# Kernel tuning notes

Measured on AMD Instinct MI355X. Metric: run time of the kernel, lower is better.

The kernel has to match this reference:

```python
import jax, jax.numpy as jnp
import numpy as np

H_BINS = 61
INSZ = 150
EPS = 1e-6


def rgb_uv_hist(img, sigma_u, sigma_v, c):
    """Differentiable RGB-uv soft histogram with per-channel RBF kernels.
    img: [B,3,H,W] in [0,1]; sigma_u, sigma_v, c: [3]. Returns [B,3,h,h]."""
    B = img.shape[0]
    x = jnp.clip(img, 0.0, 1.0).reshape(B, 3, -1)          # [B,3,P]
    Iy = jnp.sqrt(jnp.sum(x * x, axis=1))                  # [B,P] intensity weight
    lg = jnp.log(x + EPS)
    # log-chromaticity (u,v) per reference channel c in {R,G,B}
    u = jnp.stack([lg[:, 0] - lg[:, 1], lg[:, 1] - lg[:, 0], lg[:, 2] - lg[:, 0]], 1)  # [B,3,P]
    v = jnp.stack([lg[:, 0] - lg[:, 2], lg[:, 1] - lg[:, 2], lg[:, 2] - lg[:, 1]], 1)
    bins = jnp.linspace(-3.0, 3.0, H_BINS).astype(img.dtype)
    ku = jnp.exp(-((u[..., None] - bins) ** 2) / (sigma_u[None, :, None, None] ** 2))  # [B,3,P,h]
    kv = jnp.exp(-((v[..., None] - bins) ** 2) / (sigma_v[None, :, None, None] ** 2))
    w = Iy[:, None, :] * c[None, :, None]                  # [B,3,P]
    hist = jnp.einsum('bcpu,bcp,bcpv->bcuv', ku, w, kv)    # [B,3,h,h]
    norm = jnp.sum(hist, axis=(1, 2, 3), keepdims=True) + EPS
    return hist / norm


def _conv(x, w, b, stride):
    y = jax.lax.conv_general_dilated(x, w, (stride, stride), 'VALID',
                                     dimension_numbers=('NCHW', 'OIHW', 'NCHW'))
    return jax.nn.relu(y + b[None, :, None, None])


def _head(hist, w1, b1, w2, b2, w3, b3, fc):
    z = _conv(hist, w1, b1, 2)   # 61 -> 29
    z = _conv(z, w2, b2, 2)      # 29 -> 14
    z = _conv(z, w3, b3, 1)      # 14 -> 13
    z = z.reshape(z.shape[0], -1)  # [B, 512*13*13]
    return jnp.abs(z @ fc.T)


def setup_inputs() -> dict:
    key = jax.random.key(0)
    ks = jax.random.split(key, 16)
    B = 16
    d = {}
    d['image'] = jax.random.uniform(ks[0], (B, 3, INSZ, INSZ), jnp.float32)
    # hist params: sigmas in a numerically reasonable range (orig init: random()*0.02)
    d['su_s'] = 0.05 + 0.2 * jax.random.uniform(ks[1], (3,), jnp.float32)
    d['sv_s'] = 0.05 + 0.2 * jax.random.uniform(ks[2], (3,), jnp.float32)
    d['c_s'] = jnp.ones((3,), jnp.float32)
    d['w1_s'] = 0.05 * jax.random.normal(ks[3], (128, 3, 5, 5), jnp.float32)
    d['b1_s'] = jnp.zeros((128,), jnp.float32)
    d['w2_s'] = 0.02 * jax.random.normal(ks[4], (256, 128, 3, 3), jnp.float32)
    d['b2_s'] = jnp.zeros((256,), jnp.float32)
    d['w3_s'] = 0.02 * jax.random.normal(ks[5], (512, 256, 2, 2), jnp.float32)
    d['b3_s'] = jnp.zeros((512,), jnp.float32)
    d['fc_s'] = 0.003 * jax.random.normal(ks[6], (9, 512 * 13 * 13), jnp.float32)
    d['su_i'] = 0.05 + 0.2 * jax.random.uniform(ks[7], (3,), jnp.float32)
    d['sv_i'] = 0.05 + 0.2 * jax.random.uniform(ks[8], (3,), jnp.float32)
    d['c_i'] = jnp.ones((3,), jnp.float32)
    d['w1_i'] = 0.05 * jax.random.normal(ks[9], (128, 3, 5, 5), jnp.float32)
    d['b1_i'] = jnp.zeros((128,), jnp.float32)
    d['w2_i'] = 0.02 * jax.random.normal(ks[10], (256, 128, 3, 3), jnp.float32)
    d['b2_i'] = jnp.zeros((256,), jnp.float32)
    d['w3_i'] = 0.02 * jax.random.normal(ks[11], (512, 256, 2, 2), jnp.float32)
    d['b3_i'] = jnp.zeros((512,), jnp.float32)
    d['fc_i'] = 0.003 * jax.random.normal(ks[12], (3, 512 * 13 * 13), jnp.float32)
    return d


def reference(image, su_s, sv_s, c_s, w1_s, b1_s, w2_s, b2_s, w3_s, b3_s, fc_s,
              su_i, sv_i, c_i, w1_i, b1_i, w2_i, b2_i, w3_i, b3_i, fc_i):
    B = image.shape[0]
    # sensor branch: hist -> CNN -> |fc| -> 3x3 matrix (transposed), L1-row-norm scaled
    hs = rgb_uv_hist(image, su_s, sv_s, c_s)
    m = _head(hs, w1_s, b1_s, w2_s, b2_s, w3_s, b3_s, fc_s).reshape(B, 3, 3)
    m = jnp.swapaxes(m, -1, -2)                               # .t()
    n = jnp.max(jnp.sum(jnp.abs(m), axis=-1), axis=-1) + 1e-4  # max L1 row norm, [B]
    m = m / n[:, None, None]
    # color mapping: pixels @ m^T
    mapped = jnp.einsum('bjhw,bij->bihw', image, m)
    # illuminant branch on mapped image
    hi = rgb_uv_hist(mapped, su_i, sv_i, c_i)
    ill = _head(hi, w1_i, b1_i, w2_i, b2_i, w3_i, b3_i, fc_i)  # [B,3]
    est_ill = jnp.einsum('bij,bj->bi', jnp.linalg.inv(m), ill)
    return est_ill
```

## Files before the change

kernel.cpp:

```cpp
#include <hip/hip_runtime.h>

#define P_PIX 22500
#define HB 61
#define HSP 30
#define PPB 768
#define NCHK 6

typedef float f32x4 __attribute__((ext_vector_type(4)));
typedef _Float16 f16x8 __attribute__((ext_vector_type(8)));
typedef _Float16 f16x4 __attribute__((ext_vector_type(4)));

static __device__ __forceinline__ unsigned pk2(float a, float b)
{
    return __builtin_bit_cast(unsigned, __builtin_amdgcn_cvt_pkrtz(a, b));
}

static __device__ __forceinline__ float exp2_hw(float x)
{
    return __builtin_amdgcn_exp2f(x);
}

__global__ __launch_bounds__(256) void hist_mfma(
    const float* __restrict__ img, const float* __restrict__ su,
    const float* __restrict__ sv, const float* __restrict__ cw,
    const float* __restrict__ msc, float* __restrict__ hpart)
{
    const int bc = blockIdx.x;
    const int b = bc / 3, c = bc % 3;
    const int split = blockIdx.y;
    const int tid  = threadIdx.x;
    const int wv   = tid >> 6;
    const int lane = tid & 63;
    const int quad = lane >> 4;
    const int mr   = lane & 15;

    __shared__ __align__(16) _Float16 B_lds[8192];
    __shared__ __align__(16) float su_l[PPB];
    __shared__ __align__(16) float sv_l[PPB];
    __shared__ __align__(16) float sw_l[PPB];

    const float sig_u = su[c], sig_v = sv[c];
    const float L2E = 1.4426950408889634f;
    const float c1u = -L2E / (sig_u * sig_u);
    const float c1v = -L2E / (sig_v * sig_v);
    const float cwc = cw[c];
    const float ubin_b = -3.f + 0.1f * (float)lane;
    const float ubin_a = -3.f + 0.1f * (float)(wv * 16 + mr);

    const bool hasM = (msc != nullptr);
    float m00=0,m01=0,m02=0,m10=0,m11=0,m12=0,m20=0,m21=0,m22=0;
    if (hasM) {
        const float* mp = msc + b * 9;
        m00=mp[0]; m01=mp[1]; m02=mp[2];
        m10=mp[3]; m11=mp[4]; m12=mp[5];
        m20=mp[6]; m21=mp[7]; m22=mp[8];
    }

    const int p0 = split * PPB;

    for (int i = tid; i < PPB; i += 256) {
        int px = p0 + i;
        float u = 0.f, v = 0.f, wgt = 0.f;
        if (px < P_PIX) {
            const float* ip = img + (size_t)b * 3 * P_PIX + px;
            float r = ip[0], g = ip[P_PIX], bl = ip[2 * P_PIX];
            if (hasM) {
                float r2 = m00 * r + m01 * g + m02 * bl;
                float g2 = m10 * r + m11 * g + m12 * bl;
                float b2 = m20 * r + m21 * g + m22 * bl;
                r = r2; g = g2; bl = b2;
            }
            r  = fminf(fmaxf(r, 0.f), 1.f);
            g  = fminf(fmaxf(g, 0.f), 1.f);
            bl = fminf(fmaxf(bl, 0.f), 1.f);
            float Iy = sqrtf(r * r + g * g + bl * bl);
            float lr = __logf(r + 1e-6f);
            float lg = __logf(g + 1e-6f);
            float lb = __logf(bl + 1e-6f);
            if (c == 0)      { u = lr - lg; v = lr - lb; }
            else if (c == 1) { u = lg - lr; v = lg - lb; }
            else             { u = lb - lr; v = lb - lg; }
            wgt = Iy * cwc;
        }
        su_l[i] = u; sv_l[i] = v; sw_l[i] = wgt;
    }
    __syncthreads();

    f32x4 acc[4];
#pragma unroll
    for (int nt = 0; nt < 4; ++nt) acc[nt] = (f32x4){0.f, 0.f, 0.f, 0.f};

    for (int chunk = 0; chunk < NCHK; ++chunk) {
        const float* suc = &su_l[chunk * 128];
        const float* svc = &sv_l[chunk * 128];
        const float* swc = &sw_l[chunk * 128];

#pragma unroll
        for (int r = 0; r < 4; ++r) {
            int pg = wv + 4 * r;
            f32x4 v0 = *(const f32x4*)&svc[pg * 8];
            f32x4 v1 = *(const f32x4*)&svc[pg * 8 + 4];
            float e[8];
#pragma unroll
            for (int j = 0; j < 4; ++j) {
                float d0 = v0[j] - ubin_b;
                e[j] = exp2_hw((d0 * c1v) * d0);
                float d1 = v1[j] - ubin_b;
                e[4 + j] = exp2_hw((d1 * c1v) * d1);
            }
            union { f16x8 h; unsigned w[4]; } bv;
            bv.w[0] = pk2(e[0], e[1]);
            bv.w[1] = pk2(e[2], e[3]);
            bv.w[2] = pk2(e[4], e[5]);
            bv.w[3] = pk2(e[6], e[7]);
            *(f16x8*)&B_lds[(pg * 64 + lane) * 8] = bv.h;
        }
        f16x8 af[4];
#pragma unroll
        for (int kk = 0; kk < 4; ++kk) {
            int pxg = kk * 4 + quad;
            f32x4 u0 = *(const f32x4*)&suc[pxg * 8];
            f32x4 u1 = *(const f32x4*)&suc[pxg * 8 + 4];
            f32x4 w0 = *(const f32x4*)&swc[pxg * 8];
            f32x4 w1 = *(const f32x4*)&swc[pxg * 8 + 4];
            float e[8];
#pragma unroll
            for (int j = 0; j < 4; ++j) {
                float d0 = u0[j] - ubin_a;
                e[j] = exp2_hw((d0 * c1u) * d0) * w0[j];
                float d1 = u1[j] - ubin_a;
                e[4 + j] = exp2_hw((d1 * c1u) * d1) * w1[j];
            }
            union { f16x8 h; unsigned w[4]; } av;
            av.w[0] = pk2(e[0], e[1]);
            av.w[1] = pk2(e[2], e[3]);
            av.w[2] = pk2(e[4], e[5]);
            av.w[3] = pk2(e[6], e[7]);
            af[kk] = av.h;
        }
        __syncthreads();
#pragma unroll
        for (int kk = 0; kk < 4; ++kk) {
            int pgq = kk * 4 + quad;
#pragma unroll
            for (int nt = 0; nt < 4; ++nt) {
                f16x8 bvv = *(const f16x8*)&B_lds[(pgq * 64 + nt * 16 + mr) * 8];
                acc[nt] = __builtin_amdgcn_mfma_f32_16x16x32_f16(af[kk], bvv, acc[nt], 0, 0, 0);
            }
        }
        __syncthreads();
    }

    float* hp = hpart + ((size_t)bc * HSP + split) * 4096;
#pragma unroll
    for (int nt = 0; nt < 4; ++nt) {
        int v = nt * 16 + mr;
#pragma unroll
        for (int r = 0; r < 4; ++r) {
            int u = wv * 16 + quad * 4 + r;
            hp[u * 64 + v] = acc[nt][r];
        }
    }
}

__global__ __launch_bounds__(256) void reduce_hist(
    const float* __restrict__ hpart, float* __restrict__ hist,
    float* __restrict__ hsum3)
{
    const int bc = blockIdx.x;
    const int part = blockIdx.y;
    const int tid = threadIdx.x;
    const float* base = hpart + (size_t)bc * HSP * 4096;
    float lsum = 0.f;
#pragma unroll
    for (int t = 0; t < 4; ++t) {
        int idx = part * 1024 + t * 256 + tid;
        int u = idx >> 6, v = idx & 63;
        float s = 0.f;
        for (int sp = 0; sp < HSP; ++sp) s += base[sp * 4096 + idx];
        if (u < HB && v < HB) {
            hist[(size_t)bc * (HB * HB) + u * HB + v] = s;
            lsum += s;
        }
    }
    __shared__ float red[4];
    for (int off = 32; off; off >>= 1) lsum += __shfl_down(lsum, off, 64);
    if ((tid & 63) == 0) red[tid >> 6] = lsum;
    __syncthreads();
    if (tid == 0) atomicAdd(&hsum3[bc], red[0] + red[1] + red[2] + red[3]);
}

__global__ __launch_bounds__(256) void conv1_mfma(
    const float* __restrict__ hist, const float* __restrict__ hsum3,
    const _Float16* __restrict__ w1h, const float* __restrict__ bias,
    _Float16* __restrict__ out)
{
    const int b    = blockIdx.x;
    const int m0   = blockIdx.y * 64;
    const int tid  = threadIdx.x;
    const int wv   = tid >> 6;
    const int lane = tid & 63;
    const int quad = lane >> 4;
    const int mr   = lane & 15;

    __shared__ __align__(16) _Float16 A_lds[64 * 96];

    const float sc = 1.f / (hsum3[b * 3] + hsum3[b * 3 + 1] + hsum3[b * 3 + 2] + 1e-6f);
    const float* inb = hist + (size_t)b * 3 * 3721;

    for (int slot = tid; slot < 768; slot += 256) {
        int m  = slot & 63;
        int kg = slot >> 6;
        int mg = m0 + m;
        bool mok = (mg < 841);
        int oh = mok ? mg / 29 : 0;
        int ow = mok ? mg % 29 : 0;
        const float* pbase = inb + (oh * 2) * 61 + (ow * 2);
        f16x8 av;
#pragma unroll
        for (int j = 0; j < 8; ++j) {
            int k = kg * 8 + j;
            float x = 0.f;
            if (mok && k < 75) {
                int ci = k / 25, r = k % 25;
                int kh = r / 5, kw = r % 5;
                x = pbase[ci * 3721 + kh * 61 + kw] * sc;
            }
            av[j] = (_Float16)x;
        }
        *(f16x8*)&A_lds[(kg * 64 + m) * 8] = av;
    }
    __syncthreads();

    f16x8 wf[3][2];
#pragma unroll
    for (int ks = 0; ks < 3; ++ks)
#pragma unroll
        for (int nt = 0; nt < 2; ++nt) {
            int co = (wv * 2 + nt) * 16 + mr;
            wf[ks][nt] = *(const f16x8*)&w1h[co * 96 + ks * 32 + quad * 8];
        }

    f32x4 acc[4][2];
#pragma unroll
    for (int mt = 0; mt < 4; ++mt)
#pragma unroll
        for (int nt = 0; nt < 2; ++nt) acc[mt][nt] = (f32x4){0.f, 0.f, 0.f, 0.f};

#pragma unroll
    for (int ks = 0; ks < 3; ++ks)
#pragma unroll
        for (int mt = 0; mt < 4; ++mt) {
            f16x8 bv = *(const f16x8*)&A_lds[((ks * 4 + quad) * 64 + mt * 16 + mr) * 8];
#pragma unroll
            for (int nt = 0; nt < 2; ++nt)
                acc[mt][nt] = __builtin_amdgcn_mfma_f32_16x16x32_f16(bv, wf[ks][nt], acc[mt][nt], 0, 0, 0);
        }

#pragma unroll
    for (int mt = 0; mt < 4; ++mt) {
#pragma unroll
        for (int r = 0; r < 4; ++r) {
            int sp = m0 + mt * 16 + quad * 4 + r;
            if (sp >= 841) continue;
#pragma unroll
            for (int nt = 0; nt < 2; ++nt) {
                int co = (wv * 2 + nt) * 16 + mr;
                float y = acc[mt][nt][r] + bias[co];
                out[((size_t)b * 841 + sp) * 128 + co] = (_Float16)fmaxf(y, 0.f);
            }
        }
    }
}

template<int CIN, int COUT, int Kk, int S, int IN, int OUT,
         int NPB, int KSPL, int KCH, int MTILE>
__global__ __launch_bounds__(256) void conv_mfma(
    const _Float16* __restrict__ in_h,
    const _Float16* __restrict__ w_h,
    float* __restrict__ out)
{
    constexpr int KK   = Kk * Kk;
    constexpr int OSZ  = OUT * OUT;
    constexpr int MP   = MTILE;
    constexpr int MT   = MTILE / 16;
    constexpr int KTOT = CIN * KK;
    constexpr int KC   = KTOT / KSPL;
    constexpr int NCHUNK = KC / KCH;
    constexpr int NT   = NPB / 64;
    constexpr int NSPL = COUT / NPB;
    constexpr int KSN  = KCH / 32;
    constexpr int SLOTS = MP * (KCH / 8);

    const int b    = blockIdx.x;
    const int m0   = (blockIdx.y / NSPL) * MTILE;
    const int co0  = (blockIdx.y % NSPL) * NPB;
    const int k00  = blockIdx.z * KC;
    const int tid  = threadIdx.x;
    const int wv   = tid >> 6;
    const int lane = tid & 63;
    const int quad = lane >> 4;
    const int mr   = lane & 15;

    __shared__ __align__(16) _Float16 A_lds[MP * KCH];

    const _Float16* inb = in_h + (size_t)b * (IN * IN) * CIN;
    float* outp = out + (size_t)blockIdx.z * gridDim.x * OSZ * COUT;

    f32x4 acc[MT][NT];
#pragma unroll
    for (int mt = 0; mt < MT; ++mt)
#pragma unroll
        for (int nt = 0; nt < NT; ++nt) acc[mt][nt] = (f32x4){0.f, 0.f, 0.f, 0.f};

    for (int ch = 0; ch < NCHUNK; ++ch) {
        const int k0 = k00 + ch * KCH;
        __syncthreads();
        for (int slot = tid; slot < SLOTS; slot += 256) {
            int m  = slot % MP;
            int kg = slot / MP;
            int mg = m0 + m;
            bool mok = (mg < OSZ);
            int oh = mok ? mg / OUT : 0;
            int ow = mok ? mg % OUT : 0;
            int kbase = k0 + kg * 8;
            int khkw = kbase / CIN;
            int ci0  = kbase % CIN;
            int kh = khkw / Kk, kw = khkw % Kk;
            f16x8 av = (f16x8)(_Float16)0.f;
            if (mok)
                av = *(const f16x8*)&inb[((size_t)((oh * S + kh) * IN + (ow * S + kw))) * CIN + ci0];
            *(f16x8*)&A_lds[(kg * MP + m) * 8] = av;
        }
        __syncthreads();
        f16x8 wf[KSN][NT];
#pragma unroll
        for (int ks = 0; ks < KSN; ++ks)
#pragma unroll
            for (int nt = 0; nt < NT; ++nt) {
                int co = co0 + (wv * NT + nt) * 16 + mr;
                wf[ks][nt] = *(const f16x8*)&w_h[(size_t)co * KTOT + k0 + ks * 32 + quad * 8];
            }
#pragma unroll
        for (int ks = 0; ks < KSN; ++ks) {
#pragma unroll
            for (int mt = 0; mt < MT; ++mt) {
                f16x8 bv = *(const f16x8*)&A_lds[((ks * 4 + quad) * MP + mt * 16 + mr) * 8];
#pragma unroll
                for (int nt = 0; nt < NT; ++nt)
                    acc[mt][nt] = __builtin_amdgcn_mfma_f32_16x16x32_f16(bv, wf[ks][nt], acc[mt][nt], 0, 0, 0);
            }
        }
    }

#pragma unroll
    for (int mt = 0; mt < MT; ++mt) {
#pragma unroll
        for (int r = 0; r < 4; ++r) {
            int sp = m0 + mt * 16 + quad * 4 + r;
            if (sp >= OSZ) continue;
#pragma unroll
            for (int nt = 0; nt < NT; ++nt) {
                int co = co0 + (wv * NT + nt) * 16 + mr;
                outp[((size_t)b * OSZ + sp) * COUT + co] = acc[mt][nt][r];
            }
        }
    }
}

__global__ __launch_bounds__(256) void reduce_bias_relu_f16(
    const float* __restrict__ p, const float* __restrict__ bias,
    _Float16* __restrict__ out, int cout, int total4, int kspl, int total)
{
    for (int i4 = blockIdx.x * 256 + threadIdx.x; i4 < total4; i4 += gridDim.x * 256) {
        f32x4 s = (f32x4){0.f, 0.f, 0.f, 0.f};
        for (int ks = 0; ks < kspl; ++ks)
            s += *(const f32x4*)&p[(size_t)ks * total + i4 * 4];
        f32x4 bb = *(const f32x4*)&bias[(i4 * 4) % cout];
        f16x4 o;
#pragma unroll
        for (int j = 0; j < 4; ++j) o[j] = (_Float16)fmaxf(s[j] + bb[j], 0.f);
        *(f16x4*)&out[(size_t)i4 * 4] = o;
    }
}

__global__ __launch_bounds__(256) void fc_mfma(
    const _Float16* __restrict__ z, const _Float16* __restrict__ fcw,
    float* __restrict__ out, int NO)
{
    const int tid  = threadIdx.x;
    const int wv   = tid >> 6;
    const int lane = tid & 63;
    const int quad = lane >> 4;
    const int mr   = lane & 15;
    const int kw0  = blockIdx.x * 512 + wv * 128;

    __shared__ float sred[1024];

    f32x4 acc = (f32x4){0.f, 0.f, 0.f, 0.f};
    const bool bok = (mr < NO);
#pragma unroll
    for (int ks = 0; ks < 4; ++ks) {
        int kk = kw0 + ks * 32 + quad * 8;
        f16x8 av = *(const f16x8*)&z[(size_t)mr * 86528 + kk];
        f16x8 bw = (f16x8)(_Float16)0.f;
        if (bok) bw = *(const f16x8*)&fcw[(size_t)mr * 86528 + kk];
        acc = __builtin_amdgcn_mfma_f32_16x16x32_f16(av, bw, acc, 0, 0, 0);
    }
#pragma unroll
    for (int r = 0; r < 4; ++r)
        sred[wv * 256 + (quad * 4 + r) * 16 + mr] = acc[r];
    __syncthreads();
    if (tid < 256) {
        float s = sred[tid] + sred[256 + tid] + sred[512 + tid] + sred[768 + tid];
        int o = tid & 15, b = tid >> 4;
        if (o < NO) atomicAdd(&out[b * NO + o], s);
    }
}

__global__ __launch_bounds__(256) void prep_weights(
    const float* __restrict__ w1s, const float* __restrict__ w1i,
    const float* __restrict__ w2s, const float* __restrict__ w3s,
    const float* __restrict__ w2i, const float* __restrict__ w3i,
    const float* __restrict__ fcs, const float* __restrict__ fci,
    _Float16* __restrict__ w1h, _Float16* __restrict__ w23,
    _Float16* __restrict__ fch, float* __restrict__ zp)
{
    const int R0 = 384;
    const int R1 = 24576;
    const int N2 = 294912, N3 = 524288;
    const int R2 = 2 * (N2 + N3);
    const int K = 86528;
    const int R3 = 12 * K;
    const int T = R0 + R1 + R2 + R3;
    for (int i = blockIdx.x * 256 + threadIdx.x; i < T; i += gridDim.x * 256) {
        if (i < R0) {
            zp[i] = 0.f;
        } else if (i < R0 + R1) {
            int r0 = i - R0;
            int br = r0 / 12288, r = r0 % 12288;
            int co = r / 96, k = r % 96;
            const float* s = br ? w1i : w1s;
            w1h[r0] = (k < 75) ? (_Float16)s[co * 75 + k] : (_Float16)0.f;
        } else if (i < R0 + R1 + R2) {
            int j = i - R0 - R1;
            int out_idx = j;
            const float* s; int CK, KKn;
            if (j < N2)                { s = w2s; CK = 1152; KKn = 9; }
            else if (j < N2 + N3)      { s = w3s; j -= N2; CK = 1024; KKn = 4; }
            else if (j < 2 * N2 + N3)  { s = w2i; j -= N2 + N3; CK = 1152; KKn = 9; }
            else                       { s = w3i; j -= 2 * N2 + N3; CK = 1024; KKn = 4; }
            int co = j / CK, rem = j % CK;
            int ci = rem % (CK / KKn), khkw = rem / (CK / KKn);
            w23[out_idx] = (_Float16)s[co * CK + ci * KKn + khkw];
        } else {
            int j = i - R0 - R1 - R2;
            int o = j / K, rem = j % K;
            int sp = rem / 512, co = rem % 512;
            const float* s = (o < 9) ? (fcs + o * K) : (fci + (o - 9) * K);
            fch[j] = (_Float16)s[co * 169 + sp];
        }
    }
}

__global__ void build_m(const float* __restrict__ h, float* __restrict__ msc)
{
    int b = threadIdx.x;
    if (b < 16) {
        float m[9];
#pragma unroll
        for (int i = 0; i < 3; ++i)
#pragma unroll
            for (int j = 0; j < 3; ++j) m[i * 3 + j] = fabsf(h[b * 9 + j * 3 + i]);
        float n = 0.f;
#pragma unroll
        for (int i = 0; i < 3; ++i) {
            float r = m[i * 3] + m[i * 3 + 1] + m[i * 3 + 2];
            n = fmaxf(n, r);
        }
        n += 1e-4f;
        float inv = 1.f / n;
#pragma unroll
        for (int k = 0; k < 9; ++k) msc[b * 9 + k] = m[k] * inv;
    }
}

__global__ void final_est(const float* __restrict__ msc, const float* __restrict__ ill,
                          float* __restrict__ out)
{
    int bidx = threadIdx.x;
    if (bidx < 16) {
        const float* m = msc + bidx * 9;
        float a = m[0], b = m[1], c = m[2];
        float d = m[3], e = m[4], f = m[5];
        float g = m[6], h = m[7], i = m[8];
        float A = e * i - f * h, B = f * g - d * i, C = d * h - e * g;
        float D = c * h - b * i, E = a * i - c * g, F = b * g - a * h;
        float G = b * f - c * e, H = c * d - a * f, I = a * e - b * d;
        float det = a * A + b * B + c * C;
        float inv_det = 1.f / det;
        float x0 = fabsf(ill[bidx * 3 + 0]);
        float x1 = fabsf(ill[bidx * 3 + 1]);
        float x2 = fabsf(ill[bidx * 3 + 2]);
        out[bidx * 3 + 0] = (A * x0 + D * x1 + G * x2) * inv_det;
        out[bidx * 3 + 1] = (B * x0 + E * x1 + H * x2) * inv_det;
        out[bidx * 3 + 2] = (C * x0 + F * x1 + I * x2) * inv_det;
    }
}

extern "C" void kernel_launch(void* const* d_in, const int* in_sizes, int n_in,
                              void* d_out, int out_size, void* d_ws, size_t ws_size,
                              hipStream_t stream)
{
    (void)in_sizes; (void)n_in; (void)out_size; (void)ws_size;
    const float* image = (const float*)d_in[0];
    const float* su_s  = (const float*)d_in[1];
    const float* sv_s  = (const float*)d_in[2];
    const float* c_s   = (const float*)d_in[3];
    const float* w1_s  = (const float*)d_in[4];
    const float* b1_s  = (const float*)d_in[5];
    const float* w2_s  = (const float*)d_in[6];
    const float* b2_s  = (const float*)d_in[7];
    const float* w3_s  = (const float*)d_in[8];
    const float* b3_s  = (const float*)d_in[9];
    const float* fc_s  = (const float*)d_in[10];
    const float* su_i  = (const float*)d_in[11];
    const float* sv_i  = (const float*)d_in[12];
    const float* c_i   = (const float*)d_in[13];
    const float* w1_i  = (const float*)d_in[14];
    const float* b1_i  = (const float*)d_in[15];
    const float* w2_i  = (const float*)d_in[16];
    const float* b2_i  = (const float*)d_in[17];
    const float* w3_i  = (const float*)d_in[18];
    const float* b3_i  = (const float*)d_in[19];
    const float* fc_i  = (const float*)d_in[20];

    float* W      = (float*)d_ws;
    float* hist   = W;
    float* hd     = hist + 178608;
    float* hd2    = hd + 144;
    float* hsum3a = hd2 + 144;
    float* hsum3b = hsum3a + 48;
    float* msc    = hsum3b + 48;
    float* U      = msc + 144;
    float* hpart  = U;
    float* p2     = U;
    float* p3     = U;
    _Float16* o1h   = (_Float16*)(U + 11075584);
    _Float16* o2h   = o1h   + 1722368;
    _Float16* o3h   = o2h   + 802816;
    _Float16* fch   = o3h   + 1384448;
    _Float16* w2h_s = fch   + 1038336;
    _Float16* w3h_s = w2h_s + 294912;
    _Float16* w2h_i = w3h_s + 524288;
    _Float16* w3h_i = w2h_i + 294912;
    _Float16* w1h_s = w3h_i + 524288;
    _Float16* w1h_i = w1h_s + 12288;

    const int O2_TOT = 16 * 196 * 256;
    const int O3_TOT = 16 * 169 * 512;
    const int FCK = 86528;

    prep_weights<<<1024, 256, 0, stream>>>(w1_s, w1_i, w2_s, w3_s, w2_i, w3_i,
                                           fc_s, fc_i, w1h_s, w2h_s, fch, hd);

    hist_mfma<<<dim3(48, HSP), 256, 0, stream>>>(image, su_s, sv_s, c_s, nullptr, hpart);
    reduce_hist<<<dim3(48, 4), 256, 0, stream>>>(hpart, hist, hsum3a);
    conv1_mfma<<<dim3(16, 14), 256, 0, stream>>>(hist, hsum3a, w1h_s, b1_s, o1h);
    conv_mfma<128, 256, 3, 2, 29, 14, 128, 4, 96, 112><<<dim3(16, 4, 4), 256, 0, stream>>>(o1h, w2h_s, p2);
    reduce_bias_relu_f16<<<784, 256, 0, stream>>>(p2, b2_s, o2h, 256, O2_TOT / 4, 4, O2_TOT);
    conv_mfma<256, 512, 2, 1, 14, 13, 128, 2, 64, 96><<<dim3(16, 8, 2), 256, 0, stream>>>(o2h, w3h_s, p3);
    reduce_bias_relu_f16<<<1024, 256, 0, stream>>>(p3, b3_s, o3h, 512, O3_TOT / 4, 2, O3_TOT);
    fc_mfma<<<169, 256, 0, stream>>>(o3h, fch, hd, 9);
    build_m<<<1, 64, 0, stream>>>(hd, msc);

    hist_mfma<<<dim3(48, HSP), 256, 0, stream>>>(image, su_i, sv_i, c_i, msc, hpart);
    reduce_hist<<<dim3(48, 4), 256, 0, stream>>>(hpart, hist, hsum3b);
    conv1_mfma<<<dim3(16, 14), 256, 0, stream>>>(hist, hsum3b, w1h_i, b1_i, o1h);
    conv_mfma<128, 256, 3, 2, 29, 14, 128, 4, 96, 112><<<dim3(16, 4, 4), 256, 0, stream>>>(o1h, w2h_i, p2);
    reduce_bias_relu_f16<<<784, 256, 0, stream>>>(p2, b2_i, o2h, 256, O2_TOT / 4, 4, O2_TOT);
    conv_mfma<256, 512, 2, 1, 14, 13, 128, 2, 64, 96><<<dim3(16, 8, 2), 256, 0, stream>>>(o2h, w3h_i, p3);
    reduce_bias_relu_f16<<<1024, 256, 0, stream>>>(p3, b3_i, o3h, 512, O3_TOT / 4, 2, O3_TOT);
    fc_mfma<<<169, 256, 0, stream>>>(o3h, fch + 9 * FCK, hd2, 3);
    final_est<<<1, 64, 0, stream>>>(msc, hd2, (float*)d_out);
}
```

Measured before the change: 327.5 us.

## Fuse bias+ReLU into conv2/conv3 MFMA kernels and drop split-K partials

Removes the split-K decomposition of the conv2 and conv3 MFMA kernels, so each block accumulates the full K range and applies bias and ReLU before writing f16 output directly. This eliminates the fp32 partial-sum buffers and the separate reduce_bias_relu kernels, cutting four launches and their global memory round-trips. Tiles shrink to 64 output channels and 64 spatial rows per block to keep enough blocks in the grid without split-K. In exchange, each block runs a longer serial K loop and reuses the A tile across fewer output channels.

```diff
diff --git a/kernel.cpp b/kernel.cpp
--- a/kernel.cpp
+++ b/kernel.cpp
@@ -274,20 +274,19 @@
 }
 
 template<int CIN, int COUT, int Kk, int S, int IN, int OUT,
-         int NPB, int KSPL, int KCH, int MTILE>
-__global__ __launch_bounds__(256) void conv_mfma(
+         int NPB, int KCH, int MTILE>
+__global__ __launch_bounds__(256) void conv_fused_mfma(
     const _Float16* __restrict__ in_h,
     const _Float16* __restrict__ w_h,
-    float* __restrict__ out)
+    const float* __restrict__ bias,
+    _Float16* __restrict__ out)
 {
     constexpr int KK   = Kk * Kk;
     constexpr int OSZ  = OUT * OUT;
     constexpr int MP   = MTILE;
     constexpr int MT   = MTILE / 16;
     constexpr int KTOT = CIN * KK;
-    constexpr int KC   = KTOT / KSPL;
-    constexpr int NCHUNK = KC / KCH;
-    constexpr int NT   = NPB / 64;
+    constexpr int NCHUNK = KTOT / KCH;
     constexpr int NSPL = COUT / NPB;
     constexpr int KSN  = KCH / 32;
     constexpr int SLOTS = MP * (KCH / 8);
@@ -295,7 +294,6 @@
     const int b    = blockIdx.x;
     const int m0   = (blockIdx.y / NSPL) * MTILE;
     const int co0  = (blockIdx.y % NSPL) * NPB;
-    const int k00  = blockIdx.z * KC;
     const int tid  = threadIdx.x;
     const int wv   = tid >> 6;
     const int lane = tid & 63;
@@ -305,16 +303,13 @@
     __shared__ __align__(16) _Float16 A_lds[MP * KCH];
 
     const _Float16* inb = in_h + (size_t)b * (IN * IN) * CIN;
-    float* outp = out + (size_t)blockIdx.z * gridDim.x * OSZ * COUT;
-
-    f32x4 acc[MT][NT];
-#pragma unroll
-    for (int mt = 0; mt < MT; ++mt)
-#pragma unroll
-        for (int nt = 0; nt < NT; ++nt) acc[mt][nt] = (f32x4){0.f, 0.f, 0.f, 0.f};
+
+    f32x4 acc[MT];
+#pragma unroll
+    for (int mt = 0; mt < MT; ++mt) acc[mt] = (f32x4){0.f, 0.f, 0.f, 0.f};
 
     for (int ch = 0; ch < NCHUNK; ++ch) {
-        const int k0 = k00 + ch * KCH;
+        const int k0 = ch * KCH;
         __syncthreads();
         for (int slot = tid; slot < SLOTS; slot += 256) {
             int m  = slot % MP;
@@ -333,54 +328,32 @@
             *(f16x8*)&A_lds[(kg * MP + m) * 8] = av;
         }
         __syncthreads();
-        f16x8 wf[KSN][NT];
+        f16x8 wf[KSN];
+        const int co = co0 + wv * 16 + mr;
 #pragma unroll
         for (int ks = 0; ks < KSN; ++ks)
-#pragma unroll
-            for (int nt = 0; nt < NT; ++nt) {
-                int co = co0 + (wv * NT + nt) * 16 + mr;
-                wf[ks][nt] = *(const f16x8*)&w_h[(size_t)co * KTOT + k0 + ks * 32 + quad * 8];
-            }
+            wf[ks] = *(const f16x8*)&w_h[(size_t)co * KTOT + k0 + ks * 32 + quad * 8];
 #pragma unroll
         for (int ks = 0; ks < KSN; ++ks) {
 #pragma unroll
             for (int mt = 0; mt < MT; ++mt) {
                 f16x8 bv = *(const f16x8*)&A_lds[((ks * 4 + quad) * MP + mt * 16 + mr) * 8];
-#pragma unroll
-                for (int nt = 0; nt < NT; ++nt)
-                    acc[mt][nt] = __builtin_amdgcn_mfma_f32_16x16x32_f16(bv, wf[ks][nt], acc[mt][nt], 0, 0, 0);
-            }
-        }
-    }
-
+                acc[mt] = __builtin_amdgcn_mfma_f32_16x16x32_f16(bv, wf[ks], acc[mt], 0, 0, 0);
+            }
+        }
+    }
+
+    const int co = co0 + wv * 16 + mr;
+    const float bb = bias[co];
 #pragma unroll
     for (int mt = 0; mt < MT; ++mt) {
 #pragma unroll
         for (int r = 0; r < 4; ++r) {
             int sp = m0 + mt * 16 + quad * 4 + r;
             if (sp >= OSZ) continue;
-#pragma unroll
-            for (int nt = 0; nt < NT; ++nt) {
-                int co = co0 + (wv * NT + nt) * 16 + mr;
-                outp[((size_t)b * OSZ + sp) * COUT + co] = acc[mt][nt][r];
-            }
-        }
-    }
-}
-
-__global__ __launch_bounds__(256) void reduce_bias_relu_f16(
-    const float* __restrict__ p, const float* __restrict__ bias,
-    _Float16* __restrict__ out, int cout, int total4, int kspl, int total)
-{
-    for (int i4 = blockIdx.x * 256 + threadIdx.x; i4 < total4; i4 += gridDim.x * 256) {
-        f32x4 s = (f32x4){0.f, 0.f, 0.f, 0.f};
-        for (int ks = 0; ks < kspl; ++ks)
-            s += *(const f32x4*)&p[(size_t)ks * total + i4 * 4];
-        f32x4 bb = *(const f32x4*)&bias[(i4 * 4) % cout];
-        f16x4 o;
-#pragma unroll
-        for (int j = 0; j < 4; ++j) o[j] = (_Float16)fmaxf(s[j] + bb[j], 0.f);
-        *(f16x4*)&out[(size_t)i4 * 4] = o;
+            float y = acc[mt][r] + bb;
+            out[((size_t)b * OSZ + sp) * COUT + co] = (_Float16)fmaxf(y, 0.f);
+        }
     }
 }
 
@@ -544,8 +517,6 @@
     float* msc    = hsum3b + 48;
     float* U      = msc + 144;
     float* hpart  = U;
-    float* p2     = U;
-    float* p3     = U;
     _Float16* o1h   = (_Float16*)(U + 11075584);
     _Float16* o2h   = o1h   + 1722368;
     _Float16* o3h   = o2h   + 802816;
@@ -557,8 +528,6 @@
     _Float16* w1h_s = w3h_i + 524288;
     _Float16* w1h_i = w1h_s + 12288;
 
-    const int O2_TOT = 16 * 196 * 256;
-    const int O3_TOT = 16 * 169 * 512;
     const int FCK = 86528;
 
     prep_weights<<<1024, 256, 0, stream>>>(w1_s, w1_i, w2_s, w3_s, w2_i, w3_i,
@@ -567,20 +536,16 @@
     hist_mfma<<<dim3(48, HSP), 256, 0, stream>>>(image, su_s, sv_s, c_s, nullptr, hpart);
     reduce_hist<<<dim3(48, 4), 256, 0, stream>>>(hpart, hist, hsum3a);
     conv1_mfma<<<dim3(16, 14), 256, 0, stream>>>(hist, hsum3a, w1h_s, b1_s, o1h);
-    conv_mfma<128, 256, 3, 2, 29, 14, 128, 4, 96, 112><<<dim3(16, 4, 4), 256, 0, stream>>>(o1h, w2h_s, p2);
-    reduce_bias_relu_f16<<<784, 256, 0, stream>>>(p2, b2_s, o2h, 256, O2_TOT / 4, 4, O2_TOT);
-    conv_mfma<256, 512, 2, 1, 14, 13, 128, 2, 64, 96><<<dim3(16, 8, 2), 256, 0, stream>>>(o2h, w3h_s, p3);
-    reduce_bias_relu_f16<<<1024, 256, 0, stream>>>(p3, b3_s, o3h, 512, O3_TOT / 4, 2, O3_TOT);
+    conv_fused_mfma<128, 256, 3, 2, 29, 14, 64, 96, 64><<<dim3(16, 16), 256, 0, stream>>>(o1h, w2h_s, b2_s, o2h);
+    conv_fused_mfma<256, 512, 2, 1, 14, 13, 64, 64, 64><<<dim3(16, 24), 256, 0, stream>>>(o2h, w3h_s, b3_s, o3h);
     fc_mfma<<<169, 256, 0, stream>>>(o3h, fch, hd, 9);
     build_m<<<1, 64, 0, stream>>>(hd, msc);
 
     hist_mfma<<<dim3(48, HSP), 256, 0, stream>>>(image, su_i, sv_i, c_i, msc, hpart);
     reduce_hist<<<dim3(48, 4), 256, 0, stream>>>(hpart, hist, hsum3b);
     conv1_mfma<<<dim3(16, 14), 256, 0, stream>>>(hist, hsum3b, w1h_i, b1_i, o1h);
-    conv_mfma<128, 256, 3, 2, 29, 14, 128, 4, 96, 112><<<dim3(16, 4, 4), 256, 0, stream>>>(o1h, w2h_i, p2);
-    reduce_bias_relu_f16<<<784, 256, 0, stream>>>(p2, b2_i, o2h, 256, O2_TOT / 4, 4, O2_TOT);
-    conv_mfma<256, 512, 2, 1, 14, 13, 128, 2, 64, 96><<<dim3(16, 8, 2), 256, 0, stream>>>(o2h, w3h_i, p3);
-    reduce_bias_relu_f16<<<1024, 256, 0, stream>>>(p3, b3_i, o3h, 512, O3_TOT / 4, 2, O3_TOT);
+    conv_fused_mfma<128, 256, 3, 2, 29, 14, 64, 96, 64><<<dim3(16, 16), 256, 0, stream>>>(o1h, w2h_i, b2_i, o2h);
+    conv_fused_mfma<256, 512, 2, 1, 14, 13, 64, 64, 64><<<dim3(16, 24), 256, 0, stream>>>(o2h, w3h_i, b3_i, o3h);
     fc_mfma<<<169, 256, 0, stream>>>(o3h, fch + 9 * FCK, hd2, 3);
     final_est<<<1, 64, 0, stream>>>(msc, hd2, (float*)d_out);
 }
```

After: 320.5 us. 2.1% less time.
